# Kernel optimization log

Hardware: AMD Instinct MI355X
Metric: run time of the kernel (lower is better)

## Reference

```python
import jax, jax.numpy as jnp
import numpy as np

TAU = 1.5
K = 4
EPS = 1e-5
GN_GROUPS = 8

def conv2d(x, w, pad, rhs_dilation=(1, 1)):
    return jax.lax.conv_general_dilated(
        x, w, window_strides=(1, 1),
        padding=[(pad, pad), (pad, pad)],
        rhs_dilation=rhs_dilation,
        dimension_numbers=("NCHW", "OIHW", "NCHW"))

def setup_inputs() -> dict:
    key = jax.random.key(0)
    ks = jax.random.split(key, 16)
    s = 0.05  # weight scale to keep activations sane
    B, C, H, W = 16, 128, 64, 64
    O, HID, CG, SE = 128, 32, 16, 16
    d = {}
    d["x"] = jax.random.normal(ks[0], (B, C, H, W), jnp.float32)
    d["base_weight"] = jax.random.normal(ks[1], (O, C, 3, 3), jnp.float32) * s
    d["delta_weight"] = jax.random.normal(ks[2], (K, O, C, 3, 3), jnp.float32) * s
    d["kernel_scale"] = jnp.ones((K, O, 1, 1, 1), jnp.float32)
    d["gc_w1"] = jax.random.normal(ks[3], (HID, C), jnp.float32) * s
    d["gc_w2"] = jax.random.normal(ks[4], (C, HID), jnp.float32) * s
    d["rc_w"] = jax.random.normal(ks[5], (HID, C, 3, 3), jnp.float32) * s
    d["bn_gamma"] = jnp.ones((HID,), jnp.float32)
    d["bn_beta"] = jnp.zeros((HID,), jnp.float32)
    d["bn_mean"] = jnp.zeros((HID,), jnp.float32)
    d["bn_var"] = jnp.ones((HID,), jnp.float32)
    d["rg_w"] = jax.random.normal(ks[6], (HID, C), jnp.float32) * s
    d["gate_w"] = jax.random.normal(ks[7], (K * O, HID), jnp.float32) * s
    d["gate_b"] = jnp.zeros((K * O,), jnp.float32)
    d["cg_w1"] = jax.random.normal(ks[8], (CG, C), jnp.float32) * s
    d["cg_b1"] = jnp.zeros((CG,), jnp.float32)
    d["cg_w2"] = jax.random.normal(ks[9], (C, CG), jnp.float32) * s
    d["cg_b2"] = jnp.zeros((C,), jnp.float32)
    d["sg_w"] = jax.random.normal(ks[10], (1, 2, 7, 7), jnp.float32) * s
    d["gn_gamma"] = jnp.ones((O,), jnp.float32)
    d["gn_beta"] = jnp.zeros((O,), jnp.float32)
    d["se_w1"] = jax.random.normal(ks[11], (SE, O), jnp.float32) * s
    d["se_b1"] = jnp.zeros((SE,), jnp.float32)
    d["se_w2"] = jax.random.normal(ks[12], (O, SE), jnp.float32) * s
    d["se_b2"] = jnp.zeros((O,), jnp.float32)
    d["identity_scale"] = jnp.float32(0.0)
    d["bias"] = jnp.zeros((O,), jnp.float32)
    return d

def reference(x, base_weight, delta_weight, kernel_scale, gc_w1, gc_w2, rc_w,
              bn_gamma, bn_beta, bn_mean, bn_var, rg_w, gate_w, gate_b,
              cg_w1, cg_b1, cg_w2, cg_b2, sg_w, gn_gamma, gn_beta,
              se_w1, se_b1, se_w2, se_b2, identity_scale, bias):
    identity = x
    B, C, H, W = x.shape
    O = base_weight.shape[0]

    # global context gate (squeeze-excite style)
    p = x.mean((2, 3))                                    # [B,C]
    g = jax.nn.sigmoid(jax.nn.silu(p @ gc_w1.T) @ gc_w2.T)
    x = x * g[:, :, None, None]

    # channel gate
    pc = x.mean((2, 3))
    c_attn = jax.nn.sigmoid(jax.nn.silu(pc @ cg_w1.T + cg_b1) @ cg_w2.T + cg_b2)
    # spatial gate
    s_in = jnp.concatenate([x.mean(1, keepdims=True), x.max(1, keepdims=True)], axis=1)
    s_attn = jax.nn.sigmoid(conv2d(s_in, sg_w, pad=3))
    x = x * c_attn[:, :, None, None] * s_attn

    # router: dilated conv + BN(eval) + SiLU, plus global branch
    lf = conv2d(x, rc_w, pad=2, rhs_dilation=(2, 2))
    lf = (lf - bn_mean[None, :, None, None]) * jax.lax.rsqrt(bn_var + EPS)[None, :, None, None]
    lf = lf * bn_gamma[None, :, None, None] + bn_beta[None, :, None, None]
    lf = jax.nn.silu(lf)
    gf = jax.nn.silu(x.mean((2, 3)) @ rg_w.T)             # [B,HID]
    lf = lf + gf[:, :, None, None]
    alpha = jnp.einsum("bhij,oh->boij", lf, gate_w) + gate_b[None, :, None, None]
    alpha = alpha.reshape(B, K, O, H, W)
    alpha = jax.nn.softmax(alpha / TAU, axis=1)

    # unfold (k=3, stride=1, pad=1, dilation=1) -> H_out=H, W_out=W
    xp = jnp.pad(x, ((0, 0), (0, 0), (1, 1), (1, 1)))
    patches = jnp.stack([xp[:, :, i:i + H, j:j + W]
                         for i in range(3) for j in range(3)], axis=2)  # [B,C,9,H,W]
    L = H * W
    xu = patches.reshape(B, C * 9, L).transpose(0, 2, 1)  # [B,L,C*9]

    base = base_weight.reshape(O, -1)
    delta = (delta_weight * kernel_scale).reshape(K, O, -1)
    # same-size bilinear resize of alpha is the identity
    alpha_map = alpha.reshape(B, K, O, L)

    static = jnp.einsum("blf,of->bol", xu, base)          # [B,O,L]
    res = jnp.einsum("blf,kof->bkol", xu, delta)          # [B,K,O,L]
    final = static + (res * alpha_map).sum(1)
    out = final.reshape(B, O, H, W)

    # GroupNorm
    go = out.reshape(B, GN_GROUPS, O // GN_GROUPS, H, W)
    mu = go.mean((2, 3, 4), keepdims=True)
    var = go.var((2, 3, 4), keepdims=True)
    out = ((go - mu) * jax.lax.rsqrt(var + EPS)).reshape(B, O, H, W)
    out = out * gn_gamma[None, :, None, None] + gn_beta[None, :, None, None]

    # output SE
    ps = out.mean((2, 3))
    se = jax.nn.sigmoid(jax.nn.silu(ps @ se_w1.T + se_b1) @ se_w2.T + se_b2)
    out = out * se[:, :, None, None]

    out = out + jnp.tanh(identity_scale) * identity
    out = out + bias[None, :, None, None]
    return out
```

## Files before the change

### kernel.cpp

```cpp
#include <hip/hip_runtime.h>
#include <hip/hip_bf16.h>
#include <math.h>

typedef __bf16 bf16_t;
typedef __bf16 bf16x8 __attribute__((ext_vector_type(8)));
typedef __bf16 bf16x4 __attribute__((ext_vector_type(4)));
typedef float  f32x4  __attribute__((ext_vector_type(4)));

#define EPSF 1e-5f
#define TAUF 1.5f

__device__ __forceinline__ float sigmoidf_(float x){ return 1.f/(1.f+__expf(-x)); }
__device__ __forceinline__ float siluf_(float x){ return x*sigmoidf_(x); }

__device__ __forceinline__ void gload_lds16(const void* g, void* l){
  __builtin_amdgcn_global_load_lds((const __attribute__((address_space(1))) unsigned int*)g,
                                   (__attribute__((address_space(3))) unsigned int*)l, 16, 0, 0);
}

__global__ void k_pool(const float* __restrict__ x, float* __restrict__ p){
  int bc = blockIdx.x; const float* xr = x + (size_t)bc*4096;
  float s = 0.f;
  for (int i = threadIdx.x; i < 4096; i += 256) s += xr[i];
  __shared__ float sb[4];
  for (int off=32; off; off>>=1) s += __shfl_down(s, off);
  if ((threadIdx.x & 63)==0) sb[threadIdx.x>>6] = s;
  __syncthreads();
  if (threadIdx.x==0) p[bc] = (sb[0]+sb[1]+sb[2]+sb[3]) * (1.f/4096.f);
}

__global__ void k_small1(const float* __restrict__ p, const float* __restrict__ gc_w1,
                         const float* __restrict__ gc_w2, const float* __restrict__ cg_w1,
                         const float* __restrict__ cg_b1, const float* __restrict__ cg_w2,
                         const float* __restrict__ cg_b2,
                         float* __restrict__ gbuf, float* __restrict__ gate){
  int b = blockIdx.x; int t = threadIdx.x;
  __shared__ float ps[128], h1[32], pc[128], c1[16];
  ps[t] = p[b*128+t];
  __syncthreads();
  if (t < 32){ float a=0.f; for(int c=0;c<128;c++) a += ps[c]*gc_w1[t*128+c]; h1[t]=siluf_(a); }
  __syncthreads();
  float a=0.f; for(int j=0;j<32;j++) a += h1[j]*gc_w2[t*32+j];
  float g = sigmoidf_(a);
  gbuf[b*128+t] = g; pc[t] = ps[t]*g;
  __syncthreads();
  if (t < 16){ float a2=cg_b1[t]; for(int c=0;c<128;c++) a2 += pc[c]*cg_w1[t*128+c]; c1[t]=siluf_(a2); }
  __syncthreads();
  float a3=cg_b2[t]; for(int j=0;j<16;j++) a3 += c1[j]*cg_w2[t*16+j];
  gate[b*128+t] = g * sigmoidf_(a3);
}

__global__ void k_spatial(const float* __restrict__ x, const float* __restrict__ gbuf,
                          float* __restrict__ sin_){
  int bi = blockIdx.x; int b = bi>>6; int h = bi&63;
  int wv = threadIdx.x>>6, w = threadIdx.x&63;
  __shared__ float psum[4][64], pmax[4][64];
  float sm=0.f, mx=-1e30f;
  const float* xb = x + (((size_t)b*128 + wv*32)*64 + h)*64 + w;
  const float* gb = gbuf + b*128 + wv*32;
  #pragma unroll 4
  for (int c=0;c<32;c++){
    float v = xb[(size_t)c*4096] * gb[c];
    sm += v; mx = fmaxf(mx, v);
  }
  psum[wv][w]=sm; pmax[wv][w]=mx;
  __syncthreads();
  if (threadIdx.x < 64){
    float s = psum[0][w]+psum[1][w]+psum[2][w]+psum[3][w];
    float m = fmaxf(fmaxf(pmax[0][w],pmax[1][w]),fmaxf(pmax[2][w],pmax[3][w]));
    sin_[b*8192 + h*64 + w]        = s*(1.f/128.f);
    sin_[b*8192 + 4096 + h*64 + w] = m;
  }
}

__global__ void __launch_bounds__(256) k_x2(
    const float* __restrict__ x, const float* __restrict__ gate,
    const float* __restrict__ sin_, const float* __restrict__ sg_w,
    bf16_t* __restrict__ x2q, float* __restrict__ pc2){
  int bi = blockIdx.x; int b = bi>>6; int h = bi&63;
  __shared__ float tile[128*65];
  __shared__ float sh_sin[980];
  __shared__ float sh_sgw[98];
  __shared__ float satt_row[64];
  int tid = threadIdx.x, wv = tid>>6, lane = tid&63;
  for (int i=tid;i<980;i+=256){
    int c2 = i/490; int rr = i - c2*490; int r = rr/70; int k = rr - r*70;
    int hh = h + r - 3; int ww = k - 3;
    float v = 0.f;
    if (hh>=0 && hh<64 && ww>=0 && ww<64) v = sin_[b*8192 + c2*4096 + hh*64 + ww];
    sh_sin[i] = v;
  }
  if (tid < 98) sh_sgw[tid] = sg_w[tid];
  __syncthreads();
  if (tid < 64){
    float a = 0.f;
    #pragma unroll
    for (int c2=0;c2<2;c2++)
      #pragma unroll
      for (int r=0;r<7;r++)
        #pragma unroll
        for (int j=0;j<7;j++)
          a += sh_sin[c2*490 + r*70 + tid + j] * sh_sgw[c2*49 + r*7 + j];
    satt_row[tid] = sigmoidf_(a);
  }
  __syncthreads();
  float sa = satt_row[lane];
  const float* xb = x + (((size_t)b*128 + wv*32)*64 + h)*64 + lane;
  const float* gb = gate + b*128 + wv*32;
  #pragma unroll 8
  for (int i=0;i<32;i++)
    tile[(wv*32+i)*65 + lane] = xb[(size_t)i*4096] * gb[i] * sa;
  __syncthreads();
  for (int it=0; it<4; it++){
    int idx = it*256 + tid;
    int cq = idx>>6; int w = idx&63;
    int c0 = cq*8;
    bf16x8 v;
    #pragma unroll
    for (int e=0;e<8;e++) v[e] = (bf16_t)tile[(c0+e)*65 + w];
    *(bf16x8*)(x2q + (((((size_t)b*4 + (cq>>2))*4 + (cq&3))*68 + (h+2))*68 + (w+2))*8) = v;
  }
  if (tid < 128){
    const float* row = &tile[tid*65];
    float s = 0.f;
    #pragma unroll 8
    for (int w=0;w<64;w++) s += row[w];
    atomicAdd(&pc2[b*128+tid], s);
  }
}

__global__ void k_wprep(const float* __restrict__ base_w, const float* __restrict__ delta_w,
                        const float* __restrict__ kscale, const float* __restrict__ rc_w,
                        bf16_t* __restrict__ WCQ, bf16_t* __restrict__ RCWQ,
                        bf16_t* __restrict__ x2q){
  int bx = blockIdx.x;
  if (bx >= 2448){
    int p = bx - 2448;
    size_t base = (size_t)p*68*68*8;
    float4 z = {0.f,0.f,0.f,0.f};
    for (int i = threadIdx.x; i < 272; i += 256){
      int r = i/68; int wp = i - r*68;
      int hp = (r&1) + (r>>1)*66;
      *(float4*)(x2q + base + ((size_t)hp*68 + wp)*8) = z;
    }
    {
      int i = threadIdx.x;
      int hp = 2 + (i>>2);
      int wp = (i&1) + (i&2)*33;
      *(float4*)(x2q + base + ((size_t)hp*68 + wp)*8) = z;
    }
    return;
  }
  int i = bx*256 + threadIdx.x;
  if (i < 589824){
    int c8 = i&7; int o16 = (i>>3)&15; int q = (i>>7)&3; int s = (i>>9)&3;
    int h2 = (i>>11)&3; int r = i>>13; int t = r%9; int ob = r/9;
    int o = ob*16 + o16; int c = h2*32 + q*8 + c8;
    float v = base_w[(o*128+c)*9 + t] + delta_w[(((s*128)+o)*128 + c)*9 + t]*kscale[s*128+o];
    WCQ[i] = (bf16_t)v;
  } else if (i < 589824 + 36864){
    int j = i - 589824;
    int c8 = j&7; int h16 = (j>>3)&15; int q = (j>>7)&3; int n2 = (j>>9)&1;
    int r = j>>10; int t = r%9; int h2 = r/9;
    int hid = n2*16 + h16; int c = h2*32 + q*8 + c8;
    RCWQ[j] = (bf16_t)rc_w[(hid*128+c)*9 + t];
  }
}

__global__ void __launch_bounds__(256) k_router(
    const bf16_t* __restrict__ x2q, const bf16_t* __restrict__ RCWQ,
    const float* __restrict__ bn_gamma, const float* __restrict__ bn_beta,
    const float* __restrict__ bn_mean, const float* __restrict__ bn_var,
    const float* __restrict__ pc2, const float* __restrict__ rg_w,
    bf16_t* __restrict__ lfb){
  __shared__ __align__(16) char smem[44544];
  __shared__ float sgf[32];
  __shared__ float spart[256];
  int tid = threadIdx.x;
  int wv = tid>>6, lane = tid&63, m16 = lane&15, q = lane>>4;
  int rb = blockIdx.x & 31, b = blockIdx.x >> 5;
  int r0 = rb*2;
  int rloc = wv&1;
  int ws0 = (wv>>1)*2;

  {
    int hid = tid&31, seg = tid>>5;
    float a=0.f;
    #pragma unroll
    for (int j=0;j<16;j++) a += pc2[b*128 + seg*16 + j]*rg_w[hid*128 + seg*16 + j];
    spart[tid] = a;
  }

  f32x4 acc[2][2] = {};

  #pragma unroll 1
  for (int h2=0; h2<4; h2++){
    const char* asrc = (const char*)(x2q + ((((size_t)(b*4+h2)*4 + wv)*68 + r0)*68)*8);
    #pragma unroll
    for (int j=0;j<7;j++){
      if (j*64 + lane < 408)
        gload_lds16(asrc + j*1024 + lane*16, (char*)smem + wv*6528 + j*1024);
    }
    const char* wsrc = (const char*)(RCWQ + (size_t)h2*9216) + wv*4608;
    #pragma unroll
    for (int j=0;j<5;j++){
      if (j*64 + lane < 288)
        gload_lds16(wsrc + j*1024 + lane*16, (char*)smem + 26112 + wv*4608 + j*1024);
    }
    __syncthreads();
    if (h2==0 && tid < 32){
      float s = 0.f;
      #pragma unroll
      for (int k=0;k<8;k++) s += spart[k*32+tid];
      sgf[tid] = siluf_(s*(1.f/4096.f));
    }
    #pragma unroll
    for (int t=0; t<9; t++){
      int di = t/3, dj = t - di*3;
      bf16x8 aw0 = *(const bf16x8*)((const char*)smem + 26112 + (t*2+0)*1024 + q*256 + m16*16);
      bf16x8 aw1 = *(const bf16x8*)((const char*)smem + 26112 + (t*2+1)*1024 + q*256 + m16*16);
      #pragma unroll
      for (int mt=0; mt<2; mt++){
        int wseg = ws0 + mt;
        bf16x8 bs = *(const bf16x8*)((const char*)smem + q*6528 +
                     ((rloc + 2*di)*68 + wseg*16 + m16 + 2*dj)*16);
        acc[0][mt] = __builtin_amdgcn_mfma_f32_16x16x32_bf16(aw0, bs, acc[0][mt], 0,0,0);
        acc[1][mt] = __builtin_amdgcn_mfma_f32_16x16x32_bf16(aw1, bs, acc[1][mt], 0,0,0);
      }
    }
    __syncthreads();
  }

  #pragma unroll
  for (int n2=0;n2<2;n2++){
    float aa[4], bb[4];
    #pragma unroll
    for (int i=0;i<4;i++){
      int hid = n2*16 + q*4 + i;
      float a = bn_gamma[hid]*rsqrtf(bn_var[hid]+EPSF);
      aa[i] = a;
      bb[i] = bn_beta[hid] - bn_mean[hid]*a;
    }
    #pragma unroll
    for (int mt=0;mt<2;mt++){
      bf16x4 yv;
      #pragma unroll
      for (int i=0;i<4;i++){
        int hid = n2*16 + q*4 + i;
        yv[i] = (bf16_t)(siluf_(aa[i]*acc[n2][mt][i] + bb[i]) + sgf[hid]);
      }
      size_t pos = (size_t)b*4096 + (r0+rloc)*64 + (ws0+mt)*16 + m16;
      *(bf16x4*)(lfb + pos*32 + n2*16 + q*4) = yv;
    }
  }
}

__global__ void __launch_bounds__(256, 2) k_main(
    const bf16_t* __restrict__ x2q, const bf16_t* __restrict__ WCQ,
    const bf16_t* __restrict__ lfb, const float* __restrict__ gate_w,
    const float* __restrict__ gate_b, bf16_t* __restrict__ outp,
    float* __restrict__ csum, float* __restrict__ cssq){
  __shared__ __align__(16) char smem[80960];
  bf16_t* shGW  = (bf16_t*)(smem + 43584);
  float*  sred  = (float*)(smem + 80448);

  int tid = threadIdx.x;
  int wv = tid>>6, lane = tid&63, m16 = lane&15, q = lane>>4;
  int bx = blockIdx.x;
  int ob = bx >> 7; int rem = bx & 127; int b = rem >> 3; int hb = rem & 7;
  int h0 = hb*8, obase = ob*16;

  f32x4 acc[8][4] = {};

  int baseA[8];
  #pragma unroll
  for (int mi=0;mi<8;mi++){
    int row = wv*2 + (mi>>2); int wseg = mi&3;
    baseA[mi] = (row*68 + wseg*16 + m16 + 1)*16 + q*10896;
  }
  int baseB = q*256 + m16*16;

  #pragma unroll 1
  for (int h2=0; h2<4; h2++){
    const char* asrc = (const char*)(x2q + ((((size_t)(b*4+h2)*4 + wv)*68 + (h0+1))*68)*8);
    #pragma unroll
    for (int j=0;j<11;j++){
      if (j*64 + lane < 680)
        gload_lds16(asrc + j*1024 + lane*16, (char*)smem + wv*10896 + j*1024);
    }
    const char* bsrc = (const char*)WCQ + ((size_t)(ob*9)*4 + h2)*4096;
    #pragma unroll
    for (int j=0;j<9;j++)
      gload_lds16(bsrc + j*16384 + wv*1024 + lane*16,
                  (char*)smem + 43584 + j*4096 + wv*1024);
    __syncthreads();
    #pragma unroll
    for (int t=0; t<9; t++){
      int di = t/3, dj = t - di*3;
      int toff = (di*68 + dj)*16;
      bf16x8 av[8], bv[4];
      #pragma unroll
      for (int mi=0;mi<8;mi++) av[mi] = *(const bf16x8*)((const char*)smem + baseA[mi] + toff);
      #pragma unroll
      for (int s=0;s<4;s++)  bv[s] = *(const bf16x8*)((const char*)smem + 43584 + t*4096 + s*1024 + baseB);
      #pragma unroll
      for (int s=0;s<4;s++){
        #pragma unroll
        for (int mi=0;mi<8;mi++)
          acc[mi][s] = __builtin_amdgcn_mfma_f32_16x16x32_bf16(av[mi], bv[s], acc[mi][s], 0,0,0);
      }
    }
    __syncthreads();
  }

  const char* lfsrc = (const char*)(lfb + ((size_t)b*4096 + h0*64)*32);
  for (int i = wv; i < 32; i += 4)
    gload_lds16(lfsrc + i*1024 + lane*16, (char*)smem + i*1024);
  for (int idx = tid; idx < 2048; idx += 256){
    int n = idx>>5, j = idx&31;
    shGW[n*32+j] = (bf16_t)gate_w[((n>>4)*128 + obase + (n&15))*32 + j];
  }
  __syncthreads();

  bf16x8 bg[4];
  #pragma unroll
  for (int kk=0;kk<4;kk++) bg[kk] = *(const bf16x8*)((const char*)shGW + (kk*16+m16)*64 + q*16);
  float gb[4];
  #pragma unroll
  for (int kk=0;kk<4;kk++) gb[kk] = gate_b[kk*128 + obase + m16];

  const float itau = 1.f/TAUF;
  float s1 = 0.f, s2 = 0.f;
  size_t orow = ((size_t)(b*128 + obase + m16))*4096 + h0*64;
  #pragma unroll
  for (int mi=0; mi<8; mi++){
    bf16x8 avL = *(const bf16x8*)((const char*)smem + (wv*128 + mi*16 + m16)*64 + q*16);
    f32x4 zero = {};
    f32x4 lg[4];
    #pragma unroll
    for (int kk=0;kk<4;kk++)
      lg[kk] = __builtin_amdgcn_mfma_f32_16x16x32_bf16(avL, bg[kk], zero, 0,0,0);
    bf16x4 yv;
    #pragma unroll
    for (int r=0;r<4;r++){
      float l0 = (lg[0][r]+gb[0])*itau, l1 = (lg[1][r]+gb[1])*itau;
      float l2 = (lg[2][r]+gb[2])*itau, l3 = (lg[3][r]+gb[3])*itau;
      float mx = fmaxf(fmaxf(l0,l1),fmaxf(l2,l3));
      float e0=__expf(l0-mx), e1=__expf(l1-mx), e2=__expf(l2-mx), e3=__expf(l3-mx);
      float inv = 1.f/(e0+e1+e2+e3);
      float y = (e0*acc[mi][0][r] + e1*acc[mi][1][r]
               + e2*acc[mi][2][r] + e3*acc[mi][3][r])*inv;
      s1 += y; s2 += y*y;
      yv[r] = (bf16_t)y;
    }
    *(bf16x4*)(outp + orow + wv*128 + mi*16 + q*4) = yv;
  }

  s1 += __shfl_down(s1, 32); s1 += __shfl_down(s1, 16);
  s2 += __shfl_down(s2, 32); s2 += __shfl_down(s2, 16);
  if (lane < 16){ sred[wv*16 + lane] = s1; sred[64 + wv*16 + lane] = s2; }
  __syncthreads();
  if (tid < 16){
    float a = sred[tid] + sred[16+tid] + sred[32+tid] + sred[48+tid];
    float c = sred[64+tid] + sred[80+tid] + sred[96+tid] + sred[112+tid];
    atomicAdd(&csum[b*128 + obase + tid], a);
    atomicAdd(&cssq[b*128 + obase + tid], c);
  }
}

__global__ void k_small3(const float* __restrict__ csum, const float* __restrict__ cssq,
                         const float* __restrict__ gn_gamma, const float* __restrict__ gn_beta,
                         const float* __restrict__ se_w1, const float* __restrict__ se_b1,
                         const float* __restrict__ se_w2, const float* __restrict__ se_b2,
                         float* __restrict__ sca, float* __restrict__ shb){
  int b = blockIdx.x; int o = threadIdx.x;
  __shared__ float s1[128], s2[128], gmu[8], grs[8], psl[128], t1[16];
  s1[o] = csum[b*128+o]; s2[o] = cssq[b*128+o];
  __syncthreads();
  if (o<8){
    float a=0.f,a2=0.f; for(int j=0;j<16;j++){ a+=s1[o*16+j]; a2+=s2[o*16+j]; }
    float mu = a*(1.f/65536.f); float var = a2*(1.f/65536.f) - mu*mu;
    gmu[o]=mu; grs[o]=rsqrtf(var+EPSF);
  }
  __syncthreads();
  int g = o>>4;
  psl[o] = (s1[o]*(1.f/4096.f) - gmu[g])*grs[g]*gn_gamma[o] + gn_beta[o];
  __syncthreads();
  if (o<16){ float a = se_b1[o]; for(int c=0;c<128;c++) a += psl[c]*se_w1[o*128+c]; t1[o]=siluf_(a); }
  __syncthreads();
  float a = se_b2[o]; for(int j=0;j<16;j++) a += t1[j]*se_w2[o*16+j];
  float sev = sigmoidf_(a);
  sca[b*128+o] = grs[g]*gn_gamma[o]*sev;
  shb[b*128+o] = (gn_beta[o] - gmu[g]*grs[g]*gn_gamma[o])*sev;
}

__global__ void k_final(const bf16_t* __restrict__ outp, const float* __restrict__ x,
                        const float* __restrict__ sca, const float* __restrict__ shb,
                        const float* __restrict__ bias, const float* __restrict__ iscale,
                        float* __restrict__ out){
  float ts = tanhf(iscale[0]);
  size_t i = ((size_t)blockIdx.x*256 + threadIdx.x)*8;
  int bo = (int)(i>>12); int o = bo&127;
  float A = sca[bo], Bv = shb[bo] + bias[o];
  bf16x8 ov = *(const bf16x8*)(outp + i);
  float4 x0 = *(const float4*)(x+i), x1 = *(const float4*)(x+i+4);
  float4 r0, r1;
  r0.x = (float)ov[0]*A + Bv + ts*x0.x;
  r0.y = (float)ov[1]*A + Bv + ts*x0.y;
  r0.z = (float)ov[2]*A + Bv + ts*x0.z;
  r0.w = (float)ov[3]*A + Bv + ts*x0.w;
  r1.x = (float)ov[4]*A + Bv + ts*x1.x;
  r1.y = (float)ov[5]*A + Bv + ts*x1.y;
  r1.z = (float)ov[6]*A + Bv + ts*x1.z;
  r1.w = (float)ov[7]*A + Bv + ts*x1.w;
  *(float4*)(out+i) = r0; *(float4*)(out+i+4) = r1;
}

extern "C" void kernel_launch(void* const* d_in, const int* in_sizes, int n_in,
                              void* d_out, int out_size, void* d_ws, size_t ws_size,
                              hipStream_t stream){
  const float* x      = (const float*)d_in[0];
  const float* base_w = (const float*)d_in[1];
  const float* delta_w= (const float*)d_in[2];
  const float* kscale = (const float*)d_in[3];
  const float* gc_w1  = (const float*)d_in[4];
  const float* gc_w2  = (const float*)d_in[5];
  const float* rc_w   = (const float*)d_in[6];
  const float* bn_g   = (const float*)d_in[7];
  const float* bn_b   = (const float*)d_in[8];
  const float* bn_m   = (const float*)d_in[9];
  const float* bn_v   = (const float*)d_in[10];
  const float* rg_w   = (const float*)d_in[11];
  const float* gate_w = (const float*)d_in[12];
  const float* gate_b = (const float*)d_in[13];
  const float* cg_w1  = (const float*)d_in[14];
  const float* cg_b1  = (const float*)d_in[15];
  const float* cg_w2  = (const float*)d_in[16];
  const float* cg_b2  = (const float*)d_in[17];
  const float* sg_w   = (const float*)d_in[18];
  const float* gn_g   = (const float*)d_in[19];
  const float* gn_b   = (const float*)d_in[20];
  const float* se_w1  = (const float*)d_in[21];
  const float* se_b1  = (const float*)d_in[22];
  const float* se_w2  = (const float*)d_in[23];
  const float* se_b2  = (const float*)d_in[24];
  const float* iscale = (const float*)d_in[25];
  const float* bias   = (const float*)d_in[26];
  float* out = (float*)d_out;

  char* ws = (char*)d_ws;
  size_t off = 0;
  auto alloc = [&](size_t bytes)->void*{ void* p = ws + off; off += (bytes + 255) & ~(size_t)255; return p; };
  bf16_t* X2Q = (bf16_t*)alloc(16ull*4*4*68*68*8*2);
  bf16_t* WCQ = (bf16_t*)alloc(589824ull*2);
  bf16_t* RCWQ= (bf16_t*)alloc(36864ull*2);
  bf16_t* LF  = (bf16_t*)alloc(16ull*4096*32*2);
  bf16_t* OUTP= (bf16_t*)alloc(16ull*128*4096*2);
  float* PC2  = (float*)alloc(2048*4);
  float* CSUM = (float*)alloc(2048*4);
  float* CSSQ = (float*)alloc(2048*4);
  float* P    = (float*)alloc(2048*4);
  float* GB   = (float*)alloc(2048*4);
  float* GATE = (float*)alloc(2048*4);
  float* SIN  = (float*)alloc(16ull*8192*4);
  float* SCA  = (float*)alloc(2048*4);
  float* SHB  = (float*)alloc(2048*4);

  (void)hipMemsetAsync(PC2, 0, 3*8192, stream);

  k_wprep  <<<2704, 256, 0, stream>>>(base_w, delta_w, kscale, rc_w, WCQ, RCWQ, X2Q);
  k_pool   <<<2048, 256, 0, stream>>>(x, P);
  k_small1 <<<16,   128, 0, stream>>>(P, gc_w1, gc_w2, cg_w1, cg_b1, cg_w2, cg_b2, GB, GATE);
  k_spatial<<<1024, 256, 0, stream>>>(x, GB, SIN);
  k_x2     <<<1024, 256, 0, stream>>>(x, GATE, SIN, sg_w, X2Q, PC2);
  k_router <<<512,  256, 0, stream>>>(X2Q, RCWQ, bn_g, bn_b, bn_m, bn_v, PC2, rg_w, LF);
  k_main   <<<1024, 256, 0, stream>>>(X2Q, WCQ, LF, gate_w, gate_b, OUTP, CSUM, CSSQ);
  k_small3 <<<16,   128, 0, stream>>>(CSUM, CSSQ, gn_g, gn_b, se_w1, se_b1, se_w2, se_b2, SCA, SHB);
  k_final  <<<4096, 256, 0, stream>>>(OUTP, x, SCA, SHB, bias, iscale, out);
}
```

Before: 258.3 us.

## Double-buffer A tiles and share them across two channel groups in k_main

k_main now runs 512-thread blocks, with each half of the block computing a different 16-channel output group, and the grid halves. Both halves share the same staged input tile, so activation traffic into LDS is halved. The input tile is double-buffered: the next h2 slice is prefetched with explicit vmcnt waits and raw s_barrier calls instead of full __syncthreads. LDS use doubles to about 158 KB, which allows only one block per CU, and the hand-counted vmcnt values make correctness depend on exactly how many load instructions are issued.

Result: no change. 263.4 us (+2.0%).

```diff
diff --git a/kernel.cpp b/kernel.cpp
--- a/kernel.cpp
+++ b/kernel.cpp
@@ -255,54 +255,78 @@
   }
 }
 
-__global__ void __launch_bounds__(256, 2) k_main(
+__global__ void __launch_bounds__(512, 2) k_main(
     const bf16_t* __restrict__ x2q, const bf16_t* __restrict__ WCQ,
     const bf16_t* __restrict__ lfb, const float* __restrict__ gate_w,
     const float* __restrict__ gate_b, bf16_t* __restrict__ outp,
     float* __restrict__ csum, float* __restrict__ cssq){
-  __shared__ __align__(16) char smem[80960];
-  bf16_t* shGW  = (bf16_t*)(smem + 43584);
-  float*  sred  = (float*)(smem + 80448);
+  __shared__ __align__(16) char smem[161920];
+  float* sred = (float*)(smem + 160896);
 
   int tid = threadIdx.x;
   int wv = tid>>6, lane = tid&63, m16 = lane&15, q = lane>>4;
+  int hf = wv>>2, w4 = wv&3;
   int bx = blockIdx.x;
-  int ob = bx >> 7; int rem = bx & 127; int b = rem >> 3; int hb = rem & 7;
-  int h0 = hb*8, obase = ob*16;
+  int ob2 = bx >> 7; int rem = bx & 127; int b = rem >> 3; int hb = rem & 7;
+  int h0 = hb*8;
+  int obase = (ob2*2 + hf)*16;
+
+  auto STAGE_A = [&](int h2, int bsel){
+    int quad = wv>>1, rh = wv&1;
+    const char* asrc = (const char*)(x2q + ((((size_t)(b*4+h2)*4 + quad)*68 + (h0+1+rh*5))*68)*8);
+    char* adst = (char*)smem + bsel*43584 + quad*10896 + rh*5440;
+    #pragma unroll
+    for (int j=0;j<6;j++){
+      if (j*64 + lane < 340)
+        gload_lds16(asrc + (j*64+lane)*16, adst + j*1024);
+    }
+  };
+  auto STAGE_B = [&](int h2){
+    int obh = ob2*2 + hf;
+    const char* wsrc = (const char*)WCQ + (size_t)(obh*9*4 + h2)*4096;
+    char* bdst = (char*)smem + 87168 + hf*36864 + w4*9216;
+    #pragma unroll
+    for (int j=0;j<9;j++){
+      int cc = w4*576 + j*64 + lane;
+      int tap = cc>>8, r = cc&255;
+      gload_lds16(wsrc + tap*16384 + r*16, bdst + j*1024);
+    }
+  };
 
   f32x4 acc[8][4] = {};
 
   int baseA[8];
   #pragma unroll
   for (int mi=0;mi<8;mi++){
-    int row = wv*2 + (mi>>2); int wseg = mi&3;
-    baseA[mi] = (row*68 + wseg*16 + m16 + 1)*16 + q*10896;
+    int row = w4*2 + (mi>>2); int wseg = mi&3;
+    baseA[mi] = q*10896 + (row*68 + wseg*16 + m16 + 1)*16;
   }
   int baseB = q*256 + m16*16;
+
+  STAGE_A(0, 0);
+  STAGE_B(0);
 
   #pragma unroll 1
   for (int h2=0; h2<4; h2++){
-    const char* asrc = (const char*)(x2q + ((((size_t)(b*4+h2)*4 + wv)*68 + (h0+1))*68)*8);
-    #pragma unroll
-    for (int j=0;j<11;j++){
-      if (j*64 + lane < 680)
-        gload_lds16(asrc + j*1024 + lane*16, (char*)smem + wv*10896 + j*1024);
-    }
-    const char* bsrc = (const char*)WCQ + ((size_t)(ob*9)*4 + h2)*4096;
-    #pragma unroll
-    for (int j=0;j<9;j++)
-      gload_lds16(bsrc + j*16384 + wv*1024 + lane*16,
-                  (char*)smem + 43584 + j*4096 + wv*1024);
-    __syncthreads();
+    if (h2 < 3){
+      STAGE_A(h2+1, (h2+1)&1);
+      asm volatile("s_waitcnt vmcnt(6)" ::: "memory");
+    } else {
+      asm volatile("s_waitcnt vmcnt(0)" ::: "memory");
+    }
+    __builtin_amdgcn_s_barrier();
+
+    const char* Ab = (const char*)smem + (h2&1)*43584;
+    const char* Bb = (const char*)smem + 87168 + hf*36864;
     #pragma unroll
     for (int t=0; t<9; t++){
       int di = t/3, dj = t - di*3;
       int toff = (di*68 + dj)*16;
       bf16x8 av[8], bv[4];
       #pragma unroll
-      for (int mi=0;mi<8;mi++) av[mi] = *(const bf16x8*)((const char*)smem + baseA[mi] + toff);
-      #pragma unroll
-      for (int s=0;s<4;s++)  bv[s] = *(const bf16x8*)((const char*)smem + 43584 + t*4096 + s*1024 + baseB);
+      for (int mi=0;mi<8;mi++) av[mi] = *(const bf16x8*)(Ab + baseA[mi] + toff);
+      #pragma unroll
+      for (int s=0;s<4;s++)  bv[s] = *(const bf16x8*)(Bb + t*4096 + s*1024 + baseB);
       #pragma unroll
       for (int s=0;s<4;s++){
         #pragma unroll
@@ -310,21 +334,25 @@
           acc[mi][s] = __builtin_amdgcn_mfma_f32_16x16x32_bf16(av[mi], bv[s], acc[mi][s], 0,0,0);
       }
     }
-    __syncthreads();
+    __builtin_amdgcn_s_barrier();
+    if (h2 < 3) STAGE_B(h2+1);
   }
 
   const char* lfsrc = (const char*)(lfb + ((size_t)b*4096 + h0*64)*32);
-  for (int i = wv; i < 32; i += 4)
-    gload_lds16(lfsrc + i*1024 + lane*16, (char*)smem + i*1024);
-  for (int idx = tid; idx < 2048; idx += 256){
-    int n = idx>>5, j = idx&31;
-    shGW[n*32+j] = (bf16_t)gate_w[((n>>4)*128 + obase + (n&15))*32 + j];
+  #pragma unroll
+  for (int j=0;j<4;j++)
+    gload_lds16(lfsrc + j*8192 + wv*1024 + lane*16, (char*)smem + j*8192 + wv*1024);
+  bf16_t* shGW = (bf16_t*)(smem + 32768);
+  for (int idx = tid; idx < 4096; idx += 512){
+    int hf2 = idx>>11; int n = (idx>>5)&63; int j2 = idx&31;
+    shGW[idx] = (bf16_t)gate_w[((n>>4)*128 + (ob2*2+hf2)*16 + (n&15))*32 + j2];
   }
   __syncthreads();
 
   bf16x8 bg[4];
   #pragma unroll
-  for (int kk=0;kk<4;kk++) bg[kk] = *(const bf16x8*)((const char*)shGW + (kk*16+m16)*64 + q*16);
+  for (int kk=0;kk<4;kk++)
+    bg[kk] = *(const bf16x8*)((const char*)shGW + hf*4096 + (kk*16+m16)*64 + q*16);
   float gb[4];
   #pragma unroll
   for (int kk=0;kk<4;kk++) gb[kk] = gate_b[kk*128 + obase + m16];
@@ -334,7 +362,7 @@
   size_t orow = ((size_t)(b*128 + obase + m16))*4096 + h0*64;
   #pragma unroll
   for (int mi=0; mi<8; mi++){
-    bf16x8 avL = *(const bf16x8*)((const char*)smem + (wv*128 + mi*16 + m16)*64 + q*16);
+    bf16x8 avL = *(const bf16x8*)((const char*)smem + (w4*128 + mi*16 + m16)*64 + q*16);
     f32x4 zero = {};
     f32x4 lg[4];
     #pragma unroll
@@ -353,18 +381,23 @@
       s1 += y; s2 += y*y;
       yv[r] = (bf16_t)y;
     }
-    *(bf16x4*)(outp + orow + wv*128 + mi*16 + q*4) = yv;
+    *(bf16x4*)(outp + orow + w4*128 + mi*16 + q*4) = yv;
   }
 
   s1 += __shfl_down(s1, 32); s1 += __shfl_down(s1, 16);
   s2 += __shfl_down(s2, 32); s2 += __shfl_down(s2, 16);
-  if (lane < 16){ sred[wv*16 + lane] = s1; sred[64 + wv*16 + lane] = s2; }
-  __syncthreads();
-  if (tid < 16){
-    float a = sred[tid] + sred[16+tid] + sred[32+tid] + sred[48+tid];
-    float c = sred[64+tid] + sred[80+tid] + sred[96+tid] + sred[112+tid];
-    atomicAdd(&csum[b*128 + obase + tid], a);
-    atomicAdd(&cssq[b*128 + obase + tid], c);
+  if (lane < 16){ sred[wv*16 + lane] = s1; sred[128 + wv*16 + lane] = s2; }
+  __syncthreads();
+  if (tid < 32){
+    int hf2 = tid>>4, o = tid&15;
+    float a = 0.f, c = 0.f;
+    #pragma unroll
+    for (int k=0;k<4;k++){
+      a += sred[(hf2*4+k)*16 + o];
+      c += sred[128 + (hf2*4+k)*16 + o];
+    }
+    atomicAdd(&csum[b*128 + (ob2*2+hf2)*16 + o], a);
+    atomicAdd(&cssq[b*128 + (ob2*2+hf2)*16 + o], c);
   }
 }
 
@@ -474,7 +507,7 @@
   k_spatial<<<1024, 256, 0, stream>>>(x, GB, SIN);
   k_x2     <<<1024, 256, 0, stream>>>(x, GATE, SIN, sg_w, X2Q, PC2);
   k_router <<<512,  256, 0, stream>>>(X2Q, RCWQ, bn_g, bn_b, bn_m, bn_v, PC2, rg_w, LF);
-  k_main   <<<1024, 256, 0, stream>>>(X2Q, WCQ, LF, gate_w, gate_b, OUTP, CSUM, CSSQ);
+  k_main   <<<512,  512, 0, stream>>>(X2Q, WCQ, LF, gate_w, gate_b, OUTP, CSUM, CSSQ);
   k_small3 <<<16,   128, 0, stream>>>(CSUM, CSSQ, gn_g, gn_b, se_w1, se_b1, se_w2, se_b2, SCA, SHB);
   k_final  <<<4096, 256, 0, stream>>>(OUTP, x, SCA, SHB, bias, iscale, out);
 }
```
